# Performance work log

Hardware: AMD Instinct MI355X
Metric: run time of the kernel (lower is better)

Reference implementation:

```python
import jax, jax.numpy as jnp
import numpy as np

N, E = 10000, 320000
NF, HF = 256, 256  # input_nf/output_nf, hidden_nf
EPS = 1e-8


def setup_inputs() -> dict:
    key = jax.random.key(0)
    ks = jax.random.split(key, 20)
    h = jax.random.normal(ks[0], (N, NF), jnp.float32)
    coord = jax.random.normal(ks[1], (N, 3), jnp.float32)
    edge_index = jax.random.randint(ks[2], (2, E), 0, N, jnp.int32)

    def dense(k, fan_in, fan_out, scale=None):
        s = scale if scale is not None else 1.0 / np.sqrt(fan_in)
        W = jax.random.normal(k, (fan_in, fan_out), jnp.float32) * s
        b = jnp.zeros((fan_out,), jnp.float32)
        return W, b

    We1, be1 = dense(ks[3], 2 * NF + 1, HF)   # edge_mlp layer 1
    We2, be2 = dense(ks[4], HF, HF)           # edge_mlp layer 2
    Wn1, bn1 = dense(ks[5], HF + NF, HF)      # node_mlp layer 1
    Wn2, bn2 = dense(ks[6], HF, NF)           # node_mlp layer 2
    Wc1, bc1 = dense(ks[7], HF, HF)           # coord_mlp layer 1
    Wc2, bc2 = dense(ks[8], HF, 1, scale=0.001)  # coord_mlp final, tiny init (xavier gain=0.001)
    return dict(h=h, coord=coord, edge_index=edge_index,
                We1=We1, be1=be1, We2=We2, be2=be2,
                Wn1=Wn1, bn1=bn1, Wn2=Wn2, bn2=bn2,
                Wc1=Wc1, bc1=bc1, Wc2=Wc2, bc2=bc2)


def _segment_sum(data, seg_ids, num_segments):
    return jax.ops.segment_sum(data, seg_ids, num_segments=num_segments)


def reference(h, coord, edge_index, We1, be1, We2, be2, Wn1, bn1, Wn2, bn2, Wc1, bc1, Wc2, bc2):
    row, col = edge_index[0], edge_index[1]

    # coord2radial
    coord_diff = coord[row] - coord[col]                    # [E, 3]
    radial = jnp.sum(coord_diff ** 2, axis=1, keepdims=True)  # [E, 1]

    # edge model: MLP on [h_i, h_j, ||x_i - x_j||^2]
    edge_in = jnp.concatenate([h[row], h[col], radial], axis=1)  # [E, 2*NF+1]
    e = jax.nn.silu(edge_in @ We1 + be1)
    edge_feat = jax.nn.silu(e @ We2 + be2)                  # [E, HF]

    # coord model: coord_diff * coord_mlp(edge_feat), mean-aggregated
    c = jax.nn.silu(edge_feat @ Wc1 + bc1)
    trans = coord_diff * (c @ Wc2 + bc2)                    # [E, 3]
    agg_c = _segment_sum(trans, row, coord.shape[0])
    count = _segment_sum(jnp.ones_like(trans), row, coord.shape[0])
    coord_out = coord + agg_c / jnp.clip(count, 1.0)

    # node model: sum-aggregate edge features, concat with h, MLP
    agg_h = _segment_sum(edge_feat, row, h.shape[0])        # [N, HF]
    node_in = jnp.concatenate([h, agg_h], axis=1)           # [N, HF+NF]
    n = jax.nn.silu(node_in @ Wn1 + bn1)
    h_out = n @ Wn2 + bn2                                   # [N, NF]

    return h_out, coord_out
```

## Files before the change

### kernel.cpp

```cpp
#include <hip/hip_runtime.h>
#include <hip/hip_bf16.h>

typedef __bf16 bf16;
typedef __attribute__((ext_vector_type(8))) __bf16 bf16x8;
typedef __attribute__((ext_vector_type(4))) float f32x4;

static_assert(sizeof(bf16x8) == 16, "bf16x8 must be 16B");

constexpr int N_NODES = 10000;
constexpr int N_EDGES = 320000;
constexpr int KPAD    = 264;

__device__ __forceinline__ float silu_f(float x) { return x / (1.0f + __expf(-x)); }

__device__ __forceinline__ void mfma_64x64_k256(const bf16* A, const bf16* BT, int b_stride,
                                                int r, int q, f32x4 acc[4][4]) {
  for (int k0 = 0; k0 < 256; k0 += 32) {
    bf16x8 a[4], b[4];
#pragma unroll
    for (int mi = 0; mi < 4; ++mi)
      a[mi] = *(const bf16x8*)(A + (16 * mi + r) * KPAD + k0 + q * 8);
#pragma unroll
    for (int ni = 0; ni < 4; ++ni)
      b[ni] = *(const bf16x8*)(BT + (size_t)(16 * ni + r) * b_stride + k0 + q * 8);
#pragma unroll
    for (int mi = 0; mi < 4; ++mi)
#pragma unroll
      for (int ni = 0; ni < 4; ++ni)
        acc[mi][ni] = __builtin_amdgcn_mfma_f32_16x16x32_bf16(a[mi], b[ni], acc[mi][ni], 0, 0, 0);
  }
}

__global__ __launch_bounds__(256) void prep_kernel(
    const float* __restrict__ h, const float* __restrict__ We1, const float* __restrict__ We2,
    const float* __restrict__ Wn1, const float* __restrict__ Wn2, const float* __restrict__ Wc1,
    bf16* __restrict__ Hb, bf16* __restrict__ We1T, bf16* __restrict__ Wn1T,
    bf16* __restrict__ We2T, bf16* __restrict__ Wn2T, bf16* __restrict__ Wc1T) {
  int bid = blockIdx.x, tid = threadIdx.x;
  if (bid < 10000) { int i = bid * 256 + tid; Hb[i] = (bf16)h[i]; return; }
  int t = (bid - 10000) * 256 + tid;
  if (t < 131072) { int k = t >> 8, j = t & 255; We1T[j * 512 + k] = (bf16)We1[k * 256 + j]; return; }
  t -= 131072;
  if (t < 131072) { int k = t >> 8, j = t & 255; Wn1T[j * 512 + k] = (bf16)Wn1[k * 256 + j]; return; }
  t -= 131072;
  if (t < 65536) { int k = t >> 8, j = t & 255; We2T[j * 256 + k] = (bf16)We2[k * 256 + j]; return; }
  t -= 65536;
  if (t < 65536) { int k = t >> 8, j = t & 255; Wn2T[j * 256 + k] = (bf16)Wn2[k * 256 + j]; return; }
  t -= 65536;
  if (t < 65536) { int k = t >> 8, j = t & 255; Wc1T[j * 256 + k] = (bf16)Wc1[k * 256 + j]; return; }
}

__global__ __launch_bounds__(256) void hist_kernel(const int* __restrict__ eidx, int* __restrict__ hist) {
  int e = blockIdx.x * 256 + threadIdx.x;
  if (e < N_EDGES) atomicAdd(&hist[eidx[e]], 1);
}

__global__ __launch_bounds__(256) void scan_kernel(const int* __restrict__ hist,
                                                   int* __restrict__ base, int* __restrict__ cursor) {
  __shared__ int partial[256];
  int t = threadIdx.x;
  int s = 0;
#pragma unroll 4
  for (int i = 0; i < 40; ++i) { int idx = t * 40 + i; if (idx < N_NODES) s += hist[idx]; }
  partial[t] = s;
  __syncthreads();
  if (t == 0) { int run = 0; for (int i = 0; i < 256; ++i) { int v = partial[i]; partial[i] = run; run += v; } }
  __syncthreads();
  int run = partial[t];
  for (int i = 0; i < 40; ++i) {
    int idx = t * 40 + i;
    if (idx < N_NODES) { base[idx] = run; cursor[idx] = run; run += hist[idx]; }
  }
}

__global__ __launch_bounds__(256) void scatter_kernel(const int* __restrict__ eidx, int* __restrict__ cursor,
                                                      int* __restrict__ rs, int* __restrict__ cs) {
  int e = blockIdx.x * 256 + threadIdx.x;
  if (e < N_EDGES) {
    int r = eidx[e], c = eidx[N_EDGES + e];
    int p = atomicAdd(&cursor[r], 1);
    rs[p] = r; cs[p] = c;
  }
}

__global__ __launch_bounds__(256, 2) void gemm_pq(const bf16* __restrict__ Hb,
                                                  const bf16* __restrict__ We1T,
                                                  bf16* __restrict__ P, bf16* __restrict__ Q) {
  int tid = threadIdx.x, w = tid >> 6, lane = tid & 63, r = lane & 15, q = lane >> 4;
  int m0 = blockIdx.x * 64;
  const bf16* BT = We1T + (blockIdx.y ? 256 : 0) + (size_t)(w * 64) * 512;
  bf16* OUT = blockIdx.y ? Q : P;
  f32x4 acc[4][4];
#pragma unroll
  for (int mi = 0; mi < 4; ++mi)
#pragma unroll
    for (int ni = 0; ni < 4; ++ni) acc[mi][ni] = (f32x4){0.f, 0.f, 0.f, 0.f};

  for (int k0 = 0; k0 < 256; k0 += 32) {
    bf16x8 a[4], b[4];
#pragma unroll
    for (int mi = 0; mi < 4; ++mi) {
      int m = m0 + 16 * mi + r; if (m > N_NODES - 1) m = N_NODES - 1;
      a[mi] = *(const bf16x8*)(Hb + (size_t)m * 256 + k0 + q * 8);
    }
#pragma unroll
    for (int ni = 0; ni < 4; ++ni)
      b[ni] = *(const bf16x8*)(BT + (size_t)(16 * ni + r) * 512 + k0 + q * 8);
#pragma unroll
    for (int mi = 0; mi < 4; ++mi)
#pragma unroll
      for (int ni = 0; ni < 4; ++ni)
        acc[mi][ni] = __builtin_amdgcn_mfma_f32_16x16x32_bf16(a[mi], b[ni], acc[mi][ni], 0, 0, 0);
  }
#pragma unroll
  for (int ni = 0; ni < 4; ++ni) {
    int n = w * 64 + 16 * ni + (lane & 15);
#pragma unroll
    for (int mi = 0; mi < 4; ++mi)
#pragma unroll
      for (int rg = 0; rg < 4; ++rg) {
        int m = m0 + 16 * mi + q * 4 + rg;
        if (m < N_NODES) OUT[(size_t)m * 256 + n] = (bf16)acc[mi][ni][rg];
      }
  }
}

__global__ __launch_bounds__(256, 4) void edge_kernel(
    const float* __restrict__ coord, const int* __restrict__ rs, const int* __restrict__ cs,
    const float* __restrict__ We1, const float* __restrict__ be1,
    const float* __restrict__ be2, const float* __restrict__ bc1,
    const float* __restrict__ Wc2, const float* __restrict__ bc2,
    const bf16* __restrict__ P, const bf16* __restrict__ Q,
    const bf16* __restrict__ We2T, const bf16* __restrict__ Wc1T,
    float* __restrict__ agg_h, float* __restrict__ agg_c) {
  __shared__ __align__(16) bf16 buf[64 * KPAD];
  __shared__ int s_row[64], s_col[64];
  __shared__ float s_rad[64], s_cd[64][3], s_part[64][4], s_scal[64];

  int tid = threadIdx.x;
  int e0 = blockIdx.x * 64;
  int w = tid >> 6, lane = tid & 63, r = lane & 15, q = lane >> 4;

  if (tid < 64) {
    int e = e0 + tid;
    int ri = rs[e], ci = cs[e];
    s_row[tid] = ri; s_col[tid] = ci;
    float dx = coord[3 * ri + 0] - coord[3 * ci + 0];
    float dy = coord[3 * ri + 1] - coord[3 * ci + 1];
    float dz = coord[3 * ri + 2] - coord[3 * ci + 2];
    s_cd[tid][0] = dx; s_cd[tid][1] = dy; s_cd[tid][2] = dz;
    s_rad[tid] = dx * dx + dy * dy + dz * dz;
  }
  __syncthreads();

  {
    int off = (tid & 31) * 8;
    int esub = tid >> 5;
    float wv[8], bv[8];
#pragma unroll
    for (int j = 0; j < 8; ++j) { wv[j] = We1[512 * 256 + off + j]; bv[j] = be1[off + j]; }
#pragma unroll
    for (int p = 0; p < 8; ++p) {
      int e = p * 8 + esub;
      int ri = s_row[e], ci = s_col[e];
      bf16x8 pv = *(const bf16x8*)(P + (size_t)ri * 256 + off);
      bf16x8 qv = *(const bf16x8*)(Q + (size_t)ci * 256 + off);
      float rad = s_rad[e];
      bf16x8 o;
#pragma unroll
      for (int j = 0; j < 8; ++j)
        o[j] = (bf16)silu_f((float)pv[j] + (float)qv[j] + rad * wv[j] + bv[j]);
      *(bf16x8*)(buf + e * KPAD + off) = o;
    }
  }
  __syncthreads();

  {
    f32x4 acc[4][4];
#pragma unroll
    for (int mi = 0; mi < 4; ++mi)
#pragma unroll
      for (int ni = 0; ni < 4; ++ni) acc[mi][ni] = (f32x4){0.f, 0.f, 0.f, 0.f};
    mfma_64x64_k256(buf, We2T + (size_t)(w * 64) * 256, 256, r, q, acc);
    __syncthreads();
#pragma unroll
    for (int ni = 0; ni < 4; ++ni) {
      int n = w * 64 + 16 * ni + r;
      float bv = be2[n];
#pragma unroll
      for (int mi = 0; mi < 4; ++mi)
#pragma unroll
        for (int rg = 0; rg < 4; ++rg) {
          int m = 16 * mi + q * 4 + rg;
          buf[m * KPAD + n] = (bf16)silu_f(acc[mi][ni][rg] + bv);
        }
    }
  }
  __syncthreads();

  {
    float s = 0.f;
    int cur = s_row[0];
#pragma unroll 4
    for (int e = 0; e < 64; ++e) {
      int re = s_row[e];
      if (re != cur) { atomicAdd(&agg_h[(size_t)cur * 256 + tid], s); s = 0.f; cur = re; }
      s += (float)buf[e * KPAD + tid];
    }
    atomicAdd(&agg_h[(size_t)cur * 256 + tid], s);
  }

  {
    f32x4 acc[4][4];
#pragma unroll
    for (int mi = 0; mi < 4; ++mi)
#pragma unroll
      for (int ni = 0; ni < 4; ++ni) acc[mi][ni] = (f32x4){0.f, 0.f, 0.f, 0.f};
    mfma_64x64_k256(buf, Wc1T + (size_t)(w * 64) * 256, 256, r, q, acc);
    __syncthreads();
#pragma unroll
    for (int ni = 0; ni < 4; ++ni) {
      int n = w * 64 + 16 * ni + r;
      float bv = bc1[n];
#pragma unroll
      for (int mi = 0; mi < 4; ++mi)
#pragma unroll
        for (int rg = 0; rg < 4; ++rg) {
          int m = 16 * mi + q * 4 + rg;
          buf[m * KPAD + n] = (bf16)silu_f(acc[mi][ni][rg] + bv);
        }
    }
  }
  __syncthreads();

  {
    int e = tid >> 2, p = tid & 3;
    float s = 0.f;
#pragma unroll
    for (int kk = 0; kk < 64; kk += 8) {
      bf16x8 v = *(const bf16x8*)(buf + e * KPAD + p * 64 + kk);
#pragma unroll
      for (int j = 0; j < 8; ++j) s += (float)v[j] * Wc2[p * 64 + kk + j];
    }
    s_part[e][p] = s;
  }
  __syncthreads();
  if (tid < 64)
    s_scal[tid] = s_part[tid][0] + s_part[tid][1] + s_part[tid][2] + s_part[tid][3] + bc2[0];
  __syncthreads();

  if (tid < 3) {
    float s = 0.f;
    int cur = s_row[0];
    for (int e = 0; e < 64; ++e) {
      int re = s_row[e];
      if (re != cur) { atomicAdd(&agg_c[3 * cur + tid], s); s = 0.f; cur = re; }
      s += s_cd[e][tid] * s_scal[e];
    }
    atomicAdd(&agg_c[3 * cur + tid], s);
  }
}

__global__ __launch_bounds__(256) void post_kernel(
    const float* __restrict__ agg_h, bf16* __restrict__ Ab,
    const float* __restrict__ coord, const float* __restrict__ agg_c,
    const int* __restrict__ hist, float* __restrict__ coord_out) {
  int bid = blockIdx.x, tid = threadIdx.x;
  if (bid < 10000) { int i = bid * 256 + tid; Ab[i] = (bf16)agg_h[i]; return; }
  int t = (bid - 10000) * 256 + tid;
  if (t < 30000) {
    float c = (float)hist[t / 3]; if (c < 1.f) c = 1.f;
    coord_out[t] = coord[t] + agg_c[t] / c;
  }
}

__global__ __launch_bounds__(256, 2) void node_kernel(
    const bf16* __restrict__ Hb, const bf16* __restrict__ Ab,
    const bf16* __restrict__ Wn1T, const bf16* __restrict__ Wn2T,
    const float* __restrict__ bn1, const float* __restrict__ bn2,
    float* __restrict__ h_out) {
  __shared__ __align__(16) bf16 buf[64 * KPAD];
  int tid = threadIdx.x, w = tid >> 6, lane = tid & 63, r = lane & 15, q = lane >> 4;
  int m0 = blockIdx.x * 64;
  f32x4 acc[4][4];
#pragma unroll
  for (int mi = 0; mi < 4; ++mi)
#pragma unroll
    for (int ni = 0; ni < 4; ++ni) acc[mi][ni] = (f32x4){0.f, 0.f, 0.f, 0.f};

  const bf16* BT1 = Wn1T + (size_t)(w * 64) * 512;
  for (int k0 = 0; k0 < 256; k0 += 32) {
    bf16x8 a[4], b[4];
#pragma unroll
    for (int mi = 0; mi < 4; ++mi) {
      int m = m0 + 16 * mi + r; if (m > N_NODES - 1) m = N_NODES - 1;
      a[mi] = *(const bf16x8*)(Hb + (size_t)m * 256 + k0 + q * 8);
    }
#pragma unroll
    for (int ni = 0; ni < 4; ++ni)
      b[ni] = *(const bf16x8*)(BT1 + (size_t)(16 * ni + r) * 512 + k0 + q * 8);
#pragma unroll
    for (int mi = 0; mi < 4; ++mi)
#pragma unroll
      for (int ni = 0; ni < 4; ++ni)
        acc[mi][ni] = __builtin_amdgcn_mfma_f32_16x16x32_bf16(a[mi], b[ni], acc[mi][ni], 0, 0, 0);
  }
  for (int k0 = 0; k0 < 256; k0 += 32) {
    bf16x8 a[4], b[4];
#pragma unroll
    for (int mi = 0; mi < 4; ++mi) {
      int m = m0 + 16 * mi + r; if (m > N_NODES - 1) m = N_NODES - 1;
      a[mi] = *(const bf16x8*)(Ab + (size_t)m * 256 + k0 + q * 8);
    }
#pragma unroll
    for (int ni = 0; ni < 4; ++ni)
      b[ni] = *(const bf16x8*)(BT1 + (size_t)(16 * ni + r) * 512 + 256 + k0 + q * 8);
#pragma unroll
    for (int mi = 0; mi < 4; ++mi)
#pragma unroll
      for (int ni = 0; ni < 4; ++ni)
        acc[mi][ni] = __builtin_amdgcn_mfma_f32_16x16x32_bf16(a[mi], b[ni], acc[mi][ni], 0, 0, 0);
  }
#pragma unroll
  for (int ni = 0; ni < 4; ++ni) {
    int n = w * 64 + 16 * ni + (lane & 15);
    float bv = bn1[n];
#pragma unroll
    for (int mi = 0; mi < 4; ++mi)
#pragma unroll
      for (int rg = 0; rg < 4; ++rg) {
        int m = 16 * mi + q * 4 + rg;
        buf[m * KPAD + n] = (bf16)silu_f(acc[mi][ni][rg] + bv);
      }
  }
  __syncthreads();
#pragma unroll
  for (int mi = 0; mi < 4; ++mi)
#pragma unroll
    for (int ni = 0; ni < 4; ++ni) acc[mi][ni] = (f32x4){0.f, 0.f, 0.f, 0.f};
  mfma_64x64_k256(buf, Wn2T + (size_t)(w * 64) * 256, 256, r, q, acc);
#pragma unroll
  for (int ni = 0; ni < 4; ++ni) {
    int n = w * 64 + 16 * ni + (lane & 15);
    float bv = bn2[n];
#pragma unroll
    for (int mi = 0; mi < 4; ++mi)
#pragma unroll
      for (int rg = 0; rg < 4; ++rg) {
        int m = m0 + 16 * mi + q * 4 + rg;
        if (m < N_NODES) h_out[(size_t)m * 256 + n] = acc[mi][ni][rg] + bv;
      }
  }
}

extern "C" void kernel_launch(void* const* d_in, const int* in_sizes, int n_in,
                              void* d_out, int out_size, void* d_ws, size_t ws_size,
                              hipStream_t stream) {
  const float* h     = (const float*)d_in[0];
  const float* coord = (const float*)d_in[1];
  const int*   eidx  = (const int*)d_in[2];
  const float* We1 = (const float*)d_in[3];
  const float* be1 = (const float*)d_in[4];
  const float* We2 = (const float*)d_in[5];
  const float* be2 = (const float*)d_in[6];
  const float* Wn1 = (const float*)d_in[7];
  const float* bn1 = (const float*)d_in[8];
  const float* Wn2 = (const float*)d_in[9];
  const float* bn2 = (const float*)d_in[10];
  const float* Wc1 = (const float*)d_in[11];
  const float* bc1 = (const float*)d_in[12];
  const float* Wc2 = (const float*)d_in[13];
  const float* bc2 = (const float*)d_in[14];

  char* ws = (char*)d_ws;
  float* agg_h = (float*)(ws + 0);
  float* agg_c = (float*)(ws + 10240000);
  int*   hist  = (int*)  (ws + 10360000);
  int*   base  = (int*)  (ws + 10400000);
  int*   cursor= (int*)  (ws + 10440000);
  int*   rs    = (int*)  (ws + 10480000);
  int*   cs    = (int*)  (ws + 11760000);
  bf16* Hb   = (bf16*)(ws + 13040000);
  bf16* P    = (bf16*)(ws + 18160000);
  bf16* Q    = (bf16*)(ws + 23280000);
  bf16* Ab   = (bf16*)(ws + 28400000);
  bf16* We1T = (bf16*)(ws + 33520000);
  bf16* Wn1T = (bf16*)(ws + 33782144);
  bf16* We2T = (bf16*)(ws + 34044288);
  bf16* Wn2T = (bf16*)(ws + 34175360);
  bf16* Wc1T = (bf16*)(ws + 34306432);

  float* h_out = (float*)d_out;
  float* coord_out = h_out + (size_t)N_NODES * 256;

  hipMemsetAsync(ws, 0, 10400000, stream);
  prep_kernel<<<11792, 256, 0, stream>>>(h, We1, We2, Wn1, Wn2, Wc1,
                                         Hb, We1T, Wn1T, We2T, Wn2T, Wc1T);
  hist_kernel<<<1250, 256, 0, stream>>>(eidx, hist);
  scan_kernel<<<1, 256, 0, stream>>>(hist, base, cursor);
  scatter_kernel<<<1250, 256, 0, stream>>>(eidx, cursor, rs, cs);
  gemm_pq<<<dim3(157, 2), 256, 0, stream>>>(Hb, We1T, P, Q);
  edge_kernel<<<5000, 256, 0, stream>>>(coord, rs, cs, We1, be1, be2, bc1, Wc2, bc2,
                                        P, Q, We2T, Wc1T, agg_h, agg_c);
  post_kernel<<<10118, 256, 0, stream>>>(agg_h, Ab, coord, agg_c, hist, coord_out);
  node_kernel<<<157, 256, 0, stream>>>(Hb, Ab, Wn1T, Wn2T, bn1, bn2, h_out);
}
```

Measured before the change: 472.7 us.

## Replace atomic edge aggregation with stored edge features and CSR gather in node kernel

After: 593.6 us. 1.26x slower.

```diff
diff --git a/kernel.cpp b/kernel.cpp
--- a/kernel.cpp
+++ b/kernel.cpp
@@ -83,6 +83,303 @@
   }
 }
 
+__global__ __launch_bounds__(256, 2) void gemm_pq_f32(const bf16* __restrict__ Hb,
+                                                      const bf16* __restrict__ We1T,
+                                                      const float* __restrict__ be1,
+                                                      float* __restrict__ Pf, float* __restrict__ Qf) {
+  int tid = threadIdx.x, w = tid >> 6, lane = tid & 63, r = lane & 15, q = lane >> 4;
+  int m0 = blockIdx.x * 64;
+  const bf16* BT = We1T + (blockIdx.y ? 256 : 0) + (size_t)(w * 64) * 512;
+  float* OUT = blockIdx.y ? Qf : Pf;
+  bool addb = (blockIdx.y == 0);
+  f32x4 acc[4][4];
+#pragma unroll
+  for (int mi = 0; mi < 4; ++mi)
+#pragma unroll
+    for (int ni = 0; ni < 4; ++ni) acc[mi][ni] = (f32x4){0.f, 0.f, 0.f, 0.f};
+
+  for (int k0 = 0; k0 < 256; k0 += 32) {
+    bf16x8 a[4], b[4];
+#pragma unroll
+    for (int mi = 0; mi < 4; ++mi) {
+      int m = m0 + 16 * mi + r; if (m > N_NODES - 1) m = N_NODES - 1;
+      a[mi] = *(const bf16x8*)(Hb + (size_t)m * 256 + k0 + q * 8);
+    }
+#pragma unroll
+    for (int ni = 0; ni < 4; ++ni)
+      b[ni] = *(const bf16x8*)(BT + (size_t)(16 * ni + r) * 512 + k0 + q * 8);
+#pragma unroll
+    for (int mi = 0; mi < 4; ++mi)
+#pragma unroll
+      for (int ni = 0; ni < 4; ++ni)
+        acc[mi][ni] = __builtin_amdgcn_mfma_f32_16x16x32_bf16(a[mi], b[ni], acc[mi][ni], 0, 0, 0);
+  }
+#pragma unroll
+  for (int ni = 0; ni < 4; ++ni) {
+    int n = w * 64 + 16 * ni + (lane & 15);
+    float bv = addb ? be1[n] : 0.f;
+#pragma unroll
+    for (int mi = 0; mi < 4; ++mi)
+#pragma unroll
+      for (int rg = 0; rg < 4; ++rg) {
+        int m = m0 + 16 * mi + q * 4 + rg;
+        if (m < N_NODES) OUT[(size_t)m * 256 + n] = acc[mi][ni][rg] + bv;
+      }
+  }
+}
+
+__global__ __launch_bounds__(256, 4) void edge_store_kernel(
+    const float* __restrict__ coord, const int* __restrict__ rs, const int* __restrict__ cs,
+    const float* __restrict__ We1, const float* __restrict__ be2, const float* __restrict__ bc1,
+    const float* __restrict__ Wc2, const float* __restrict__ bc2,
+    const float* __restrict__ Pf, const float* __restrict__ Qf,
+    const bf16* __restrict__ We2T, const bf16* __restrict__ Wc1T,
+    bf16* __restrict__ ef, float* __restrict__ trans) {
+  __shared__ __align__(16) bf16 buf[64 * KPAD];
+  __shared__ int s_row[64], s_col[64];
+  __shared__ float s_rad[64], s_cd[64][3], s_part[64][4];
+
+  int tid = threadIdx.x;
+  int e0 = blockIdx.x * 64;
+  int w = tid >> 6, lane = tid & 63, r = lane & 15, q = lane >> 4;
+
+  if (tid < 64) {
+    int e = e0 + tid;
+    int ri = rs[e], ci = cs[e];
+    s_row[tid] = ri; s_col[tid] = ci;
+    float dx = coord[3 * ri + 0] - coord[3 * ci + 0];
+    float dy = coord[3 * ri + 1] - coord[3 * ci + 1];
+    float dz = coord[3 * ri + 2] - coord[3 * ci + 2];
+    s_cd[tid][0] = dx; s_cd[tid][1] = dy; s_cd[tid][2] = dz;
+    s_rad[tid] = dx * dx + dy * dy + dz * dz;
+  }
+  __syncthreads();
+
+  {
+    int off = (tid & 31) * 8;
+    int esub = tid >> 5;
+    float wv[8];
+#pragma unroll
+    for (int j = 0; j < 8; ++j) wv[j] = We1[512 * 256 + off + j];
+#pragma unroll
+    for (int p = 0; p < 8; ++p) {
+      int e = p * 8 + esub;
+      int ri = s_row[e], ci = s_col[e];
+      const float* pp = Pf + (size_t)ri * 256 + off;
+      const float* qq = Qf + (size_t)ci * 256 + off;
+      float4 a0 = *(const float4*)pp, a1 = *(const float4*)(pp + 4);
+      float4 b0 = *(const float4*)qq, b1 = *(const float4*)(qq + 4);
+      float rad = s_rad[e];
+      bf16x8 o;
+      o[0] = (bf16)silu_f(a0.x + b0.x + rad * wv[0]);
+      o[1] = (bf16)silu_f(a0.y + b0.y + rad * wv[1]);
+      o[2] = (bf16)silu_f(a0.z + b0.z + rad * wv[2]);
+      o[3] = (bf16)silu_f(a0.w + b0.w + rad * wv[3]);
+      o[4] = (bf16)silu_f(a1.x + b1.x + rad * wv[4]);
+      o[5] = (bf16)silu_f(a1.y + b1.y + rad * wv[5]);
+      o[6] = (bf16)silu_f(a1.z + b1.z + rad * wv[6]);
+      o[7] = (bf16)silu_f(a1.w + b1.w + rad * wv[7]);
+      *(bf16x8*)(buf + e * KPAD + off) = o;
+    }
+  }
+  __syncthreads();
+
+  {
+    f32x4 acc[4][4];
+#pragma unroll
+    for (int mi = 0; mi < 4; ++mi)
+#pragma unroll
+      for (int ni = 0; ni < 4; ++ni) acc[mi][ni] = (f32x4){0.f, 0.f, 0.f, 0.f};
+    mfma_64x64_k256(buf, We2T + (size_t)(w * 64) * 256, 256, r, q, acc);
+    __syncthreads();
+#pragma unroll
+    for (int ni = 0; ni < 4; ++ni) {
+      int n = w * 64 + 16 * ni + r;
+      float bv = be2[n];
+#pragma unroll
+      for (int mi = 0; mi < 4; ++mi)
+#pragma unroll
+        for (int rg = 0; rg < 4; ++rg) {
+          int m = 16 * mi + q * 4 + rg;
+          buf[m * KPAD + n] = (bf16)silu_f(acc[mi][ni][rg] + bv);
+        }
+    }
+  }
+  __syncthreads();
+
+  {
+    int row = tid >> 2, c0 = (tid & 3) * 64;
+#pragma unroll
+    for (int k = 0; k < 64; k += 8) {
+      bf16x8 v = *(const bf16x8*)(buf + row * KPAD + c0 + k);
+      *(bf16x8*)(ef + (size_t)(e0 + row) * 256 + c0 + k) = v;
+    }
+  }
+
+  {
+    f32x4 acc[4][4];
+#pragma unroll
+    for (int mi = 0; mi < 4; ++mi)
+#pragma unroll
+      for (int ni = 0; ni < 4; ++ni) acc[mi][ni] = (f32x4){0.f, 0.f, 0.f, 0.f};
+    mfma_64x64_k256(buf, Wc1T + (size_t)(w * 64) * 256, 256, r, q, acc);
+    __syncthreads();
+#pragma unroll
+    for (int ni = 0; ni < 4; ++ni) {
+      int n = w * 64 + 16 * ni + r;
+      float bv = bc1[n];
+#pragma unroll
+      for (int mi = 0; mi < 4; ++mi)
+#pragma unroll
+        for (int rg = 0; rg < 4; ++rg) {
+          int m = 16 * mi + q * 4 + rg;
+          buf[m * KPAD + n] = (bf16)silu_f(acc[mi][ni][rg] + bv);
+        }
+    }
+  }
+  __syncthreads();
+
+  {
+    int e = tid >> 2, p = tid & 3;
+    float s = 0.f;
+#pragma unroll
+    for (int kk = 0; kk < 64; kk += 8) {
+      bf16x8 v = *(const bf16x8*)(buf + e * KPAD + p * 64 + kk);
+#pragma unroll
+      for (int j = 0; j < 8; ++j) s += (float)v[j] * Wc2[p * 64 + kk + j];
+    }
+    s_part[e][p] = s;
+  }
+  __syncthreads();
+  if (tid < 64) {
+    float s = s_part[tid][0] + s_part[tid][1] + s_part[tid][2] + s_part[tid][3] + bc2[0];
+    size_t t3 = (size_t)(e0 + tid) * 3;
+    trans[t3 + 0] = s_cd[tid][0] * s;
+    trans[t3 + 1] = s_cd[tid][1] * s;
+    trans[t3 + 2] = s_cd[tid][2] * s;
+  }
+}
+
+__global__ __launch_bounds__(256, 2) void agg_node_kernel(
+    const bf16* __restrict__ Hb, const bf16* __restrict__ ef, const float* __restrict__ trans,
+    const int* __restrict__ base, const int* __restrict__ endp,
+    const float* __restrict__ coord,
+    const bf16* __restrict__ Wn1T, const bf16* __restrict__ Wn2T,
+    const float* __restrict__ bn1, const float* __restrict__ bn2,
+    float* __restrict__ h_out, float* __restrict__ coord_out) {
+  __shared__ __align__(16) bf16 buf[64 * KPAD];
+  int tid = threadIdx.x, w = tid >> 6, lane = tid & 63, r = lane & 15, q = lane >> 4;
+  int m0 = blockIdx.x * 64;
+
+  {
+    int strip = tid >> 5;
+    int off = (tid & 31) * 8;
+#pragma unroll
+    for (int i = 0; i < 8; ++i) {
+      int lm = strip * 8 + i;
+      int m = m0 + lm;
+      float acc[8] = {0, 0, 0, 0, 0, 0, 0, 0};
+      if (m < N_NODES) {
+        int b = base[m], e = endp[m];
+        for (int p = b; p < e; ++p) {
+          bf16x8 v = *(const bf16x8*)(ef + (size_t)p * 256 + off);
+#pragma unroll
+          for (int j = 0; j < 8; ++j) acc[j] += (float)v[j];
+        }
+      }
+      bf16x8 o;
+#pragma unroll
+      for (int j = 0; j < 8; ++j) o[j] = (bf16)acc[j];
+      *(bf16x8*)(buf + lm * KPAD + off) = o;
+    }
+  }
+  if (tid < 64) {
+    int m = m0 + tid;
+    if (m < N_NODES) {
+      int b = base[m], e = endp[m];
+      float sx = 0.f, sy = 0.f, sz = 0.f;
+      for (int p = b; p < e; ++p) {
+        sx += trans[3 * (size_t)p + 0];
+        sy += trans[3 * (size_t)p + 1];
+        sz += trans[3 * (size_t)p + 2];
+      }
+      float c = (float)(e - b); if (c < 1.f) c = 1.f;
+      coord_out[3 * m + 0] = coord[3 * m + 0] + sx / c;
+      coord_out[3 * m + 1] = coord[3 * m + 1] + sy / c;
+      coord_out[3 * m + 2] = coord[3 * m + 2] + sz / c;
+    }
+  }
+  __syncthreads();
+
+  f32x4 acc[4][4];
+#pragma unroll
+  for (int mi = 0; mi < 4; ++mi)
+#pragma unroll
+    for (int ni = 0; ni < 4; ++ni) acc[mi][ni] = (f32x4){0.f, 0.f, 0.f, 0.f};
+  const bf16* BT1 = Wn1T + (size_t)(w * 64) * 512;
+  for (int k0 = 0; k0 < 256; k0 += 32) {
+    bf16x8 a[4], b[4];
+#pragma unroll
+    for (int mi = 0; mi < 4; ++mi) {
+      int m = m0 + 16 * mi + r; if (m > N_NODES - 1) m = N_NODES - 1;
+      a[mi] = *(const bf16x8*)(Hb + (size_t)m * 256 + k0 + q * 8);
+    }
+#pragma unroll
+    for (int ni = 0; ni < 4; ++ni)
+      b[ni] = *(const bf16x8*)(BT1 + (size_t)(16 * ni + r) * 512 + k0 + q * 8);
+#pragma unroll
+    for (int mi = 0; mi < 4; ++mi)
+#pragma unroll
+      for (int ni = 0; ni < 4; ++ni)
+        acc[mi][ni] = __builtin_amdgcn_mfma_f32_16x16x32_bf16(a[mi], b[ni], acc[mi][ni], 0, 0, 0);
+  }
+  for (int k0 = 0; k0 < 256; k0 += 32) {
+    bf16x8 a[4], b[4];
+#pragma unroll
+    for (int mi = 0; mi < 4; ++mi)
+      a[mi] = *(const bf16x8*)(buf + (16 * mi + r) * KPAD + k0 + q * 8);
+#pragma unroll
+    for (int ni = 0; ni < 4; ++ni)
+      b[ni] = *(const bf16x8*)(BT1 + (size_t)(16 * ni + r) * 512 + 256 + k0 + q * 8);
+#pragma unroll
+    for (int mi = 0; mi < 4; ++mi)
+#pragma unroll
+      for (int ni = 0; ni < 4; ++ni)
+        acc[mi][ni] = __builtin_amdgcn_mfma_f32_16x16x32_bf16(a[mi], b[ni], acc[mi][ni], 0, 0, 0);
+  }
+  __syncthreads();
+#pragma unroll
+  for (int ni = 0; ni < 4; ++ni) {
+    int n = w * 64 + 16 * ni + (lane & 15);
+    float bv = bn1[n];
+#pragma unroll
+    for (int mi = 0; mi < 4; ++mi)
+#pragma unroll
+      for (int rg = 0; rg < 4; ++rg) {
+        int m = 16 * mi + q * 4 + rg;
+        buf[m * KPAD + n] = (bf16)silu_f(acc[mi][ni][rg] + bv);
+      }
+  }
+  __syncthreads();
+#pragma unroll
+  for (int mi = 0; mi < 4; ++mi)
+#pragma unroll
+    for (int ni = 0; ni < 4; ++ni) acc[mi][ni] = (f32x4){0.f, 0.f, 0.f, 0.f};
+  mfma_64x64_k256(buf, Wn2T + (size_t)(w * 64) * 256, 256, r, q, acc);
+#pragma unroll
+  for (int ni = 0; ni < 4; ++ni) {
+    int n = w * 64 + 16 * ni + (lane & 15);
+    float bv = bn2[n];
+#pragma unroll
+    for (int mi = 0; mi < 4; ++mi)
+#pragma unroll
+      for (int rg = 0; rg < 4; ++rg) {
+        int m = m0 + 16 * mi + q * 4 + rg;
+        if (m < N_NODES) h_out[(size_t)m * 256 + n] = acc[mi][ni][rg] + bv;
+      }
+  }
+}
+
 __global__ __launch_bounds__(256, 2) void gemm_pq(const bf16* __restrict__ Hb,
                                                   const bf16* __restrict__ We1T,
                                                   bf16* __restrict__ P, bf16* __restrict__ Q) {
@@ -95,7 +392,6 @@
   for (int mi = 0; mi < 4; ++mi)
 #pragma unroll
     for (int ni = 0; ni < 4; ++ni) acc[mi][ni] = (f32x4){0.f, 0.f, 0.f, 0.f};
-
   for (int k0 = 0; k0 < 256; k0 += 32) {
     bf16x8 a[4], b[4];
 #pragma unroll
@@ -136,11 +432,9 @@
   __shared__ __align__(16) bf16 buf[64 * KPAD];
   __shared__ int s_row[64], s_col[64];
   __shared__ float s_rad[64], s_cd[64][3], s_part[64][4], s_scal[64];
-
   int tid = threadIdx.x;
   int e0 = blockIdx.x * 64;
   int w = tid >> 6, lane = tid & 63, r = lane & 15, q = lane >> 4;
-
   if (tid < 64) {
     int e = e0 + tid;
     int ri = rs[e], ci = cs[e];
@@ -152,7 +446,6 @@
     s_rad[tid] = dx * dx + dy * dy + dz * dz;
   }
   __syncthreads();
-
   {
     int off = (tid & 31) * 8;
     int esub = tid >> 5;
@@ -174,7 +467,6 @@
     }
   }
   __syncthreads();
-
   {
     f32x4 acc[4][4];
 #pragma unroll
@@ -197,7 +489,6 @@
     }
   }
   __syncthreads();
-
   {
     float s = 0.f;
     int cur = s_row[0];
@@ -209,7 +500,6 @@
     }
     atomicAdd(&agg_h[(size_t)cur * 256 + tid], s);
   }
-
   {
     f32x4 acc[4][4];
 #pragma unroll
@@ -232,7 +522,6 @@
     }
   }
   __syncthreads();
-
   {
     int e = tid >> 2, p = tid & 3;
     float s = 0.f;
@@ -248,7 +537,6 @@
   if (tid < 64)
     s_scal[tid] = s_part[tid][0] + s_part[tid][1] + s_part[tid][2] + s_part[tid][3] + bc2[0];
   __syncthreads();
-
   if (tid < 3) {
     float s = 0.f;
     int cur = s_row[0];
@@ -287,7 +575,6 @@
   for (int mi = 0; mi < 4; ++mi)
 #pragma unroll
     for (int ni = 0; ni < 4; ++ni) acc[mi][ni] = (f32x4){0.f, 0.f, 0.f, 0.f};
-
   const bf16* BT1 = Wn1T + (size_t)(w * 64) * 512;
   for (int k0 = 0; k0 < 256; k0 += 32) {
     bf16x8 a[4], b[4];
@@ -372,36 +659,66 @@
   const float* Wc2 = (const float*)d_in[13];
   const float* bc2 = (const float*)d_in[14];
 
-  char* ws = (char*)d_ws;
-  float* agg_h = (float*)(ws + 0);
-  float* agg_c = (float*)(ws + 10240000);
-  int*   hist  = (int*)  (ws + 10360000);
-  int*   base  = (int*)  (ws + 10400000);
-  int*   cursor= (int*)  (ws + 10440000);
-  int*   rs    = (int*)  (ws + 10480000);
-  int*   cs    = (int*)  (ws + 11760000);
-  bf16* Hb   = (bf16*)(ws + 13040000);
-  bf16* P    = (bf16*)(ws + 18160000);
-  bf16* Q    = (bf16*)(ws + 23280000);
-  bf16* Ab   = (bf16*)(ws + 28400000);
-  bf16* We1T = (bf16*)(ws + 33520000);
-  bf16* Wn1T = (bf16*)(ws + 33782144);
-  bf16* We2T = (bf16*)(ws + 34044288);
-  bf16* Wn2T = (bf16*)(ws + 34175360);
-  bf16* Wc1T = (bf16*)(ws + 34306432);
-
   float* h_out = (float*)d_out;
   float* coord_out = h_out + (size_t)N_NODES * 256;
-
-  hipMemsetAsync(ws, 0, 10400000, stream);
-  prep_kernel<<<11792, 256, 0, stream>>>(h, We1, We2, Wn1, Wn2, Wc1,
-                                         Hb, We1T, Wn1T, We2T, Wn2T, Wc1T);
-  hist_kernel<<<1250, 256, 0, stream>>>(eidx, hist);
-  scan_kernel<<<1, 256, 0, stream>>>(hist, base, cursor);
-  scatter_kernel<<<1250, 256, 0, stream>>>(eidx, cursor, rs, cs);
-  gemm_pq<<<dim3(157, 2), 256, 0, stream>>>(Hb, We1T, P, Q);
-  edge_kernel<<<5000, 256, 0, stream>>>(coord, rs, cs, We1, be1, be2, bc1, Wc2, bc2,
-                                        P, Q, We2T, Wc1T, agg_h, agg_c);
-  post_kernel<<<10118, 256, 0, stream>>>(agg_h, Ab, coord, agg_c, hist, coord_out);
-  node_kernel<<<157, 256, 0, stream>>>(Hb, Ab, Wn1T, Wn2T, bn1, bn2, h_out);
-}
+  char* ws = (char*)d_ws;
+
+  if (ws_size >= 197000000ull) {
+    int*   hist  = (int*)  (ws + 0);
+    int*   base  = (int*)  (ws + 40000);
+    int*   cursor= (int*)  (ws + 80000);
+    int*   rs    = (int*)  (ws + 120000);
+    int*   cs    = (int*)  (ws + 1400000);
+    bf16*  Hb    = (bf16*) (ws + 2680000);
+    float* Pf    = (float*)(ws + 7800000);
+    float* Qf    = (float*)(ws + 18040000);
+    bf16*  We1T  = (bf16*) (ws + 28280000);
+    bf16*  Wn1T  = (bf16*) (ws + 28542144);
+    bf16*  We2T  = (bf16*) (ws + 28804288);
+    bf16*  Wn2T  = (bf16*) (ws + 28935360);
+    bf16*  Wc1T  = (bf16*) (ws + 29066432);
+    float* trans = (float*)(ws + 29197504);
+    bf16*  ef    = (bf16*) (ws + 33037504);
+
+    hipMemsetAsync(hist, 0, 40000, stream);
+    prep_kernel<<<11792, 256, 0, stream>>>(h, We1, We2, Wn1, Wn2, Wc1,
+                                           Hb, We1T, Wn1T, We2T, Wn2T, Wc1T);
+    hist_kernel<<<1250, 256, 0, stream>>>(eidx, hist);
+    scan_kernel<<<1, 256, 0, stream>>>(hist, base, cursor);
+    scatter_kernel<<<1250, 256, 0, stream>>>(eidx, cursor, rs, cs);
+    gemm_pq_f32<<<dim3(157, 2), 256, 0, stream>>>(Hb, We1T, be1, Pf, Qf);
+    edge_store_kernel<<<5000, 256, 0, stream>>>(coord, rs, cs, We1, be2, bc1, Wc2, bc2,
+                                                Pf, Qf, We2T, Wc1T, ef, trans);
+    agg_node_kernel<<<157, 256, 0, stream>>>(Hb, ef, trans, base, cursor, coord,
+                                             Wn1T, Wn2T, bn1, bn2, h_out, coord_out);
+  } else {
+    float* agg_h = (float*)(ws + 0);
+    float* agg_c = (float*)(ws + 10240000);
+    int*   hist  = (int*)  (ws + 10360000);
+    int*   base  = (int*)  (ws + 10400000);
+    int*   cursor= (int*)  (ws + 10440000);
+    int*   rs    = (int*)  (ws + 10480000);
+    int*   cs    = (int*)  (ws + 11760000);
+    bf16* Hb   = (bf16*)(ws + 13040000);
+    bf16* P    = (bf16*)(ws + 18160000);
+    bf16* Q    = (bf16*)(ws + 23280000);
+    bf16* Ab   = (bf16*)(ws + 28400000);
+    bf16* We1T = (bf16*)(ws + 33520000);
+    bf16* Wn1T = (bf16*)(ws + 33782144);
+    bf16* We2T = (bf16*)(ws + 34044288);
+    bf16* Wn2T = (bf16*)(ws + 34175360);
+    bf16* Wc1T = (bf16*)(ws + 34306432);
+
+    hipMemsetAsync(ws, 0, 10400000, stream);
+    prep_kernel<<<11792, 256, 0, stream>>>(h, We1, We2, Wn1, Wn2, Wc1,
+                                           Hb, We1T, Wn1T, We2T, Wn2T, Wc1T);
+    hist_kernel<<<1250, 256, 0, stream>>>(eidx, hist);
+    scan_kernel<<<1, 256, 0, stream>>>(hist, base, cursor);
+    scatter_kernel<<<1250, 256, 0, stream>>>(eidx, cursor, rs, cs);
+    gemm_pq<<<dim3(157, 2), 256, 0, stream>>>(Hb, We1T, P, Q);
+    edge_kernel<<<5000, 256, 0, stream>>>(coord, rs, cs, We1, be1, be2, bc1, Wc2, bc2,
+                                          P, Q, We2T, Wc1T, agg_h, agg_c);
+    post_kernel<<<10118, 256, 0, stream>>>(agg_h, Ab, coord, agg_c, hist, coord_out);
+    node_kernel<<<157, 256, 0, stream>>>(Hb, Ab, Wn1T, Wn2T, bn1, bn2, h_out);
+  }
+}
```
